# Performance work log

Hardware: AMD Instinct MI355X
Metric: run time of the kernel (lower is better)

Reference implementation:

```python
import math
import jax, jax.numpy as jnp
import numpy as np

NUM_HEADS = 16
D_MODEL = 1024
B, S = 1, 4096


def setup_inputs() -> dict:
    key = jax.random.key(0)
    ks = jax.random.split(key, 10)
    sc = 1.0 / math.sqrt(D_MODEL)
    # causal mask: 1.0 where masked (strictly upper triangular), 0.0 elsewhere
    causal = jnp.triu(jnp.ones((S, S), dtype=jnp.float32), k=1)
    return {
        "query": jax.random.normal(ks[0], (B, S, D_MODEL), dtype=jnp.float32),
        "mask": jnp.broadcast_to(causal, (B, S, S)),
        "Wq": jax.random.normal(ks[1], (D_MODEL, D_MODEL), dtype=jnp.float32) * sc,
        "bq": jax.random.normal(ks[2], (D_MODEL,), dtype=jnp.float32) * sc,
        "Wk": jax.random.normal(ks[3], (D_MODEL, D_MODEL), dtype=jnp.float32) * sc,
        "bk": jax.random.normal(ks[4], (D_MODEL,), dtype=jnp.float32) * sc,
        "Wv": jax.random.normal(ks[5], (D_MODEL, D_MODEL), dtype=jnp.float32) * sc,
        "bv": jax.random.normal(ks[6], (D_MODEL,), dtype=jnp.float32) * sc,
        "Wo": jax.random.normal(ks[7], (D_MODEL, D_MODEL), dtype=jnp.float32) * sc,
        "bo": jax.random.normal(ks[8], (D_MODEL,), dtype=jnp.float32) * sc,
    }


def _split_heads(x, H, dh):
    # [B,S,D] -> [B,H,S,dh]; head h owns channels [h*dh:(h+1)*dh] (matches the
    # module's transpose->reshape->transpose trick, which equals the contiguous split)
    b, s, _ = x.shape
    return x.reshape(b, s, H, dh).transpose(0, 2, 1, 3)


def reference(query, mask, Wq, bq, Wk, bk, Wv, bv, Wo, bo):
    H = NUM_HEADS
    B_, S_, D = query.shape
    dh = D // H
    q = _split_heads(query @ Wq.T + bq, H, dh)   # [B,H,S,dh]
    k = _split_heads(query @ Wk.T + bk, H, dh)   # self-attention: key = query
    v = _split_heads(query @ Wv.T + bv, H, dh)
    # materialized scores [B,H,S,S]
    scores = jnp.einsum("bhqd,bhkd->bhqk", q, k)
    # mask applied BEFORE the 1/sqrt(d_head) scaling, faithful to the source
    scores = scores + mask[:, None, :, :] * (-1e9)
    attn = jax.nn.softmax(scores / math.sqrt(dh), axis=-1)  # [B,H,S,S]
    out = jnp.einsum("bhqk,bhkd->bhqd", attn, v)            # [B,H,S,dh]
    combined = out.transpose(0, 2, 1, 3).reshape(B_, S_, D)  # [B,S,D]
    return combined @ Wo.T + bo
```

## Files before the change

kernel.cpp:

```cpp
#include <hip/hip_runtime.h>

typedef __bf16 bf16x8 __attribute__((ext_vector_type(8)));
typedef __bf16 bf16x4 __attribute__((ext_vector_type(4)));
typedef float f32x4 __attribute__((ext_vector_type(4)));

typedef const __attribute__((address_space(1))) void* as1_cvp;
typedef __attribute__((address_space(3))) void* as3_vp;
__device__ __forceinline__ void g2l16(const void* g, void* l) {
  __builtin_amdgcn_global_load_lds((as1_cvp)(uintptr_t)g, (as3_vp)(uintptr_t)l, 16, 0, 0);
}

__global__ __launch_bounds__(256) void cast_f32_to_bf16(const float* __restrict__ in,
                                                        __bf16* __restrict__ out, int n4) {
  for (int idx = blockIdx.x * 256 + threadIdx.x; idx < n4; idx += gridDim.x * 256) {
    float4 f = reinterpret_cast<const float4*>(in)[idx];
    bf16x4 t;
    t.x = (__bf16)f.x; t.y = (__bf16)f.y; t.z = (__bf16)f.z; t.w = (__bf16)f.w;
    reinterpret_cast<bf16x4*>(out)[idx] = t;
  }
}

__global__ __launch_bounds__(256) void cast3_f32_to_bf16(const float* __restrict__ w0,
                                                         const float* __restrict__ w1,
                                                         const float* __restrict__ w2,
                                                         __bf16* __restrict__ out, int n4,
                                                         float qs) {
  const float* src = blockIdx.y == 0 ? w0 : (blockIdx.y == 1 ? w1 : w2);
  const float s = blockIdx.y == 0 ? qs : 1.0f;
  __bf16* dst = out + (size_t)blockIdx.y * (size_t)n4 * 4;
  for (int idx = blockIdx.x * 256 + threadIdx.x; idx < n4; idx += gridDim.x * 256) {
    float4 f = reinterpret_cast<const float4*>(src)[idx];
    bf16x4 t;
    t.x = (__bf16)(f.x * s); t.y = (__bf16)(f.y * s);
    t.z = (__bf16)(f.z * s); t.w = (__bf16)(f.w * s);
    reinterpret_cast<bf16x4*>(dst)[idx] = t;
  }
}

template <int BM, typename OUT_T, bool VT_FUSE>
__global__ __launch_bounds__(256) void gemm_bt(const __bf16* __restrict__ A,
                                               const __bf16* __restrict__ B,
                                               const float* __restrict__ b0,
                                               const float* __restrict__ b1,
                                               const float* __restrict__ b2,
                                               OUT_T* __restrict__ C,
                                               __bf16* __restrict__ Vt,
                                               int K, int ldc, float qs) {
  constexpr int MT = BM / 32;
  __shared__ __align__(16) __bf16 Alds[BM][64];
  __shared__ __align__(16) __bf16 Blds[128][64];
  const int tid = threadIdx.x;
  const int wave = tid >> 6, lane = tid & 63;
  const int wm = wave & 1, wn = wave >> 1;
  const int mlane = lane & 15, quad = lane >> 4;
  const int m0 = blockIdx.x * BM, n0 = blockIdx.y * 128;

  f32x4 acc[MT][4] = {};
  constexpr int AN = BM * 8 / 256;

  for (int k0 = 0; k0 < K; k0 += 64) {
#pragma unroll
    for (int j = 0; j < AN; j++) {
      int c = j * 256 + tid;
      g2l16(&A[(size_t)(m0 + (c >> 3)) * K + k0 + (c & 7) * 8], &Alds[0][0] + c * 8);
    }
#pragma unroll
    for (int j = 0; j < 4; j++) {
      int c = j * 256 + tid;
      g2l16(&B[(size_t)(n0 + (c >> 3)) * K + k0 + (c & 7) * 8], &Blds[0][0] + c * 8);
    }
    __syncthreads();
    bf16x8 af[MT][2], bfr[4][2];
#pragma unroll
    for (int mt = 0; mt < MT; mt++)
#pragma unroll
      for (int s = 0; s < 2; s++)
        af[mt][s] = *reinterpret_cast<const bf16x8*>(
            &Alds[wm * (BM / 2) + mt * 16 + mlane][s * 32 + quad * 8]);
#pragma unroll
    for (int nt = 0; nt < 4; nt++)
#pragma unroll
      for (int s = 0; s < 2; s++)
        bfr[nt][s] = *reinterpret_cast<const bf16x8*>(
            &Blds[wn * 64 + nt * 16 + mlane][s * 32 + quad * 8]);
#pragma unroll
    for (int mt = 0; mt < MT; mt++)
#pragma unroll
      for (int nt = 0; nt < 4; nt++)
#pragma unroll
        for (int s = 0; s < 2; s++)
          acc[mt][nt] = __builtin_amdgcn_mfma_f32_16x16x32_bf16(af[mt][s], bfr[nt][s],
                                                                acc[mt][nt], 0, 0, 0);
    __syncthreads();
  }

  const int region = n0 >> 10;
  const float* bp = region == 0 ? b0 : (region == 1 ? b1 : b2);
  const float bs = (region == 0) ? qs : 1.0f;
  float bvs[4];
#pragma unroll
  for (int nt = 0; nt < 4; nt++)
    bvs[nt] = bp[(n0 + wn * 64 + nt * 16 + mlane) & 1023] * bs;

  if (VT_FUSE && region == 2) {
#pragma unroll
    for (int mt = 0; mt < MT; mt++)
#pragma unroll
      for (int nt = 0; nt < 4; nt++) {
        int vcol = ((n0 + wn * 64 + nt * 16 + mlane) & 1023);
        int row0 = m0 + wm * (BM / 2) + mt * 16 + quad * 4;
        bf16x4 t;
#pragma unroll
        for (int r = 0; r < 4; r++) t[r] = (__bf16)(acc[mt][nt][r] + bvs[nt]);
        *reinterpret_cast<bf16x4*>(&Vt[(size_t)vcol * 4096 + row0]) = t;
      }
  } else {
#pragma unroll
    for (int mt = 0; mt < MT; mt++)
#pragma unroll
      for (int nt = 0; nt < 4; nt++) {
        int col = n0 + wn * 64 + nt * 16 + mlane;
#pragma unroll
        for (int r = 0; r < 4; r++) {
          int row = m0 + wm * (BM / 2) + mt * 16 + quad * 4 + r;
          C[(size_t)row * ldc + col] = (OUT_T)(acc[mt][nt][r] + bvs[nt]);
        }
      }
  }
}

__global__ __launch_bounds__(512, 4) void flash_attn(const __bf16* __restrict__ QK,
                                                     const __bf16* __restrict__ Vt,
                                                     __bf16* __restrict__ O, int S) {
  const int LDQ = 2048, D = 1024;
  __shared__ __align__(16) __bf16 Klds[128][72];
  __shared__ __align__(16) __bf16 Vlds[64][136];
  __shared__ __align__(16) __bf16 Plds[8][16][72];
  const int tid = threadIdx.x;
  const int wave = tid >> 6, lane = tid & 63;
  const int mlane = lane & 15, quad = lane >> 4;
  const int half = wave >> 2, rw = wave & 3;
  const int b = blockIdx.x, h = blockIdx.y;

  for (int pass = 0; pass < 2; ++pass) {
    const int qb = pass ? b : (63 - b);
    const int qbase = qb * 64 + rw * 16;

    bf16x8 qf[2];
#pragma unroll
    for (int s = 0; s < 2; s++)
      qf[s] = *reinterpret_cast<const bf16x8*>(
          &QK[(size_t)(qbase + mlane) * LDQ + h * 64 + s * 32 + quad * 8]);

    f32x4 o[4] = {};
    float lrow[4] = {0.f, 0.f, 0.f, 0.f};

    const int nkb = qb / 2 + 1;
    for (int kb = 0; kb < nkb; ++kb) {
#pragma unroll
      for (int j = 0; j < 2; j++) {
        int c = j * 512 + tid, r = c >> 3, cc = c & 7;
        *reinterpret_cast<uint4*>(&Klds[r][cc * 8]) = *reinterpret_cast<const uint4*>(
            &QK[(size_t)(kb * 128 + r) * LDQ + 1024 + h * 64 + cc * 8]);
      }
#pragma unroll
      for (int j = 0; j < 2; j++) {
        int c = j * 512 + tid, r = c >> 4, cc = c & 15;
        *reinterpret_cast<uint4*>(&Vlds[r][cc * 8]) = *reinterpret_cast<const uint4*>(
            &Vt[(size_t)(h * 64 + r) * S + kb * 128 + cc * 8]);
      }
      __syncthreads();

      f32x4 sc[4];
#pragma unroll
      for (int nt = 0; nt < 4; nt++) {
        f32x4 a = {};
#pragma unroll
        for (int s = 0; s < 2; s++) {
          bf16x8 bk = *reinterpret_cast<const bf16x8*>(
              &Klds[half * 64 + nt * 16 + mlane][s * 32 + quad * 8]);
          a = __builtin_amdgcn_mfma_f32_16x16x32_bf16(qf[s], bk, a, 0, 0, 0);
        }
        sc[nt] = a;
      }

      const bool maskTile = (kb == nkb - 1);
#pragma unroll
      for (int r = 0; r < 4; r++) {
        if (maskTile) {
          const int qg = qbase + quad * 4 + r;
#pragma unroll
          for (int nt = 0; nt < 4; nt++) {
            int kg = kb * 128 + half * 64 + nt * 16 + mlane;
            if (kg > qg) sc[nt][r] = -INFINITY;
          }
        }
        float ls = 0.f;
#pragma unroll
        for (int nt = 0; nt < 4; nt++) {
          float p = __builtin_amdgcn_exp2f(sc[nt][r]);
          sc[nt][r] = p;
          ls += p;
        }
        lrow[r] += ls;
#pragma unroll
        for (int nt = 0; nt < 4; nt++)
          Plds[wave][quad * 4 + r][nt * 16 + mlane] = (__bf16)sc[nt][r];
      }

#pragma unroll
      for (int s = 0; s < 2; s++) {
        bf16x8 pf =
            *reinterpret_cast<const bf16x8*>(&Plds[wave][mlane][s * 32 + quad * 8]);
#pragma unroll
        for (int nt = 0; nt < 4; nt++) {
          bf16x8 vf = *reinterpret_cast<const bf16x8*>(
              &Vlds[nt * 16 + mlane][half * 64 + s * 32 + quad * 8]);
          o[nt] = __builtin_amdgcn_mfma_f32_16x16x32_bf16(pf, vf, o[nt], 0, 0, 0);
        }
      }
      __syncthreads();
    }

    float* osc = (float*)&Klds[0][0];
    float* lsc = (float*)&Vlds[0][0];
    if (half == 1) {
      const int ob = (rw * 64 + lane) * 18, lb = (rw * 64 + lane) * 5;
#pragma unroll
      for (int nt = 0; nt < 4; nt++)
#pragma unroll
        for (int r = 0; r < 4; r++) osc[ob + nt * 4 + r] = o[nt][r];
#pragma unroll
      for (int r = 0; r < 4; r++) lsc[lb + r] = lrow[r];
    }
    __syncthreads();
    if (half == 0) {
      const int ob = (rw * 64 + lane) * 18, lb = (rw * 64 + lane) * 5;
#pragma unroll
      for (int nt = 0; nt < 4; nt++)
#pragma unroll
        for (int r = 0; r < 4; r++) o[nt][r] += osc[ob + nt * 4 + r];
#pragma unroll
      for (int r = 0; r < 4; r++) {
        float l = lrow[r] + lsc[lb + r];
#pragma unroll
        for (int off = 1; off < 16; off <<= 1) l += __shfl_xor(l, off, 64);
        float inv = 1.0f / l;
        int row = qbase + quad * 4 + r;
#pragma unroll
        for (int nt = 0; nt < 4; nt++)
          O[(size_t)row * D + h * 64 + nt * 16 + mlane] = (__bf16)(o[nt][r] * inv);
      }
    }
    __syncthreads();
  }
}

extern "C" void kernel_launch(void* const* d_in, const int* in_sizes, int n_in,
                              void* d_out, int out_size, void* d_ws, size_t ws_size,
                              hipStream_t stream) {
  const float* query = (const float*)d_in[0];
  const float* Wq = (const float*)d_in[2];
  const float* bq = (const float*)d_in[3];
  const float* Wk = (const float*)d_in[4];
  const float* bk = (const float*)d_in[5];
  const float* Wv = (const float*)d_in[6];
  const float* bv = (const float*)d_in[7];
  const float* Wo = (const float*)d_in[8];
  const float* bo = (const float*)d_in[9];
  float* out = (float*)d_out;

  const int S = 4096, D = 1024;
  const float SCL = 0.125f * 1.44269504088896340736f;
  char* ws = (char*)d_ws;
  __bf16* Xb   = (__bf16*)(ws);
  __bf16* Cb   = (__bf16*)(ws);
  __bf16* Wqkv = (__bf16*)(ws + (8u << 20));
  __bf16* Wob  = (__bf16*)(ws + (14u << 20));
  __bf16* QKb  = (__bf16*)(ws + (16u << 20));
  __bf16* Vt   = (__bf16*)(ws + (32u << 20));

  cast_f32_to_bf16<<<1024, 256, 0, stream>>>(query, Xb, S * D / 4);
  cast3_f32_to_bf16<<<dim3(256, 3), 256, 0, stream>>>(Wq, Wk, Wv, Wqkv, D * D / 4, SCL);
  cast_f32_to_bf16<<<256, 256, 0, stream>>>(Wo, Wob, D * D / 4);

  gemm_bt<128, __bf16, true><<<dim3(S / 128, 3 * D / 128), 256, 0, stream>>>(
      Xb, Wqkv, bq, bk, bv, QKb, Vt, D, 2048, SCL);

  flash_attn<<<dim3(32, 16), 512, 0, stream>>>(QKb, Vt, Cb, S);

  gemm_bt<64, float, false><<<dim3(S / 64, D / 128), 256, 0, stream>>>(
      Cb, Wob, bo, bo, bo, out, nullptr, D, D, 1.0f);
}
```

Measured before the change: 283.5 us.

## Prefetch next K/V tile into registers and retune LDS padding

The attention kernel now loads the next K and V tiles from global memory into registers while the current tile is being computed. At the top of each iteration it only stores those registers into LDS, so global-load latency overlaps with the MFMA and softmax work. The LDS row padding is also cut (72→68, 136→132, reduction stride 18→17) to change the bank mapping. With the new padding, row strides are no longer 16-byte multiples, so the 128-bit LDS accesses may become misaligned. The prefetch also holds extra registers per thread.

```diff
diff --git a/kernel.cpp b/kernel.cpp
--- a/kernel.cpp
+++ b/kernel.cpp
@@ -133,15 +133,18 @@
                                                      const __bf16* __restrict__ Vt,
                                                      __bf16* __restrict__ O, int S) {
   const int LDQ = 2048, D = 1024;
-  __shared__ __align__(16) __bf16 Klds[128][72];
-  __shared__ __align__(16) __bf16 Vlds[64][136];
-  __shared__ __align__(16) __bf16 Plds[8][16][72];
+  __shared__ __align__(16) __bf16 Klds[128][68];
+  __shared__ __align__(16) __bf16 Vlds[64][132];
+  __shared__ __align__(16) __bf16 Plds[8][16][68];
   const int tid = threadIdx.x;
   const int wave = tid >> 6, lane = tid & 63;
   const int mlane = lane & 15, quad = lane >> 4;
   const int half = wave >> 2, rw = wave & 3;
   const int b = blockIdx.x, h = blockIdx.y;
 
+  const int krow = tid >> 3, kcol = (tid & 7) * 8;
+  const int vrow = tid >> 4, vcol = (tid & 15) * 8;
+
   for (int pass = 0; pass < 2; ++pass) {
     const int qb = pass ? b : (63 - b);
     const int qbase = qb * 64 + rw * 16;
@@ -156,20 +159,37 @@
     float lrow[4] = {0.f, 0.f, 0.f, 0.f};
 
     const int nkb = qb / 2 + 1;
+
+    uint4 kreg[2], vreg[2];
+#pragma unroll
+    for (int j = 0; j < 2; j++)
+      kreg[j] = *reinterpret_cast<const uint4*>(
+          &QK[(size_t)(j * 64 + krow) * LDQ + 1024 + h * 64 + kcol]);
+#pragma unroll
+    for (int j = 0; j < 2; j++)
+      vreg[j] = *reinterpret_cast<const uint4*>(
+          &Vt[(size_t)(h * 64 + j * 32 + vrow) * S + vcol]);
+
     for (int kb = 0; kb < nkb; ++kb) {
 #pragma unroll
-      for (int j = 0; j < 2; j++) {
-        int c = j * 512 + tid, r = c >> 3, cc = c & 7;
-        *reinterpret_cast<uint4*>(&Klds[r][cc * 8]) = *reinterpret_cast<const uint4*>(
-            &QK[(size_t)(kb * 128 + r) * LDQ + 1024 + h * 64 + cc * 8]);
-      }
-#pragma unroll
-      for (int j = 0; j < 2; j++) {
-        int c = j * 512 + tid, r = c >> 4, cc = c & 15;
-        *reinterpret_cast<uint4*>(&Vlds[r][cc * 8]) = *reinterpret_cast<const uint4*>(
-            &Vt[(size_t)(h * 64 + r) * S + kb * 128 + cc * 8]);
-      }
+      for (int j = 0; j < 2; j++)
+        *reinterpret_cast<uint4*>(&Klds[j * 64 + krow][kcol]) = kreg[j];
+#pragma unroll
+      for (int j = 0; j < 2; j++)
+        *reinterpret_cast<uint4*>(&Vlds[j * 32 + vrow][vcol]) = vreg[j];
       __syncthreads();
+
+      if (kb + 1 < nkb) {
+        const int kb2 = kb + 1;
+#pragma unroll
+        for (int j = 0; j < 2; j++)
+          kreg[j] = *reinterpret_cast<const uint4*>(
+              &QK[(size_t)(kb2 * 128 + j * 64 + krow) * LDQ + 1024 + h * 64 + kcol]);
+#pragma unroll
+        for (int j = 0; j < 2; j++)
+          vreg[j] = *reinterpret_cast<const uint4*>(
+              &Vt[(size_t)(h * 64 + j * 32 + vrow) * S + kb2 * 128 + vcol]);
+      }
 
       f32x4 sc[4];
 #pragma unroll
@@ -225,7 +245,7 @@
     float* osc = (float*)&Klds[0][0];
     float* lsc = (float*)&Vlds[0][0];
     if (half == 1) {
-      const int ob = (rw * 64 + lane) * 18, lb = (rw * 64 + lane) * 5;
+      const int ob = (rw * 64 + lane) * 17, lb = (rw * 64 + lane) * 5;
 #pragma unroll
       for (int nt = 0; nt < 4; nt++)
 #pragma unroll
@@ -235,7 +255,7 @@
     }
     __syncthreads();
     if (half == 0) {
-      const int ob = (rw * 64 + lane) * 18, lb = (rw * 64 + lane) * 5;
+      const int ob = (rw * 64 + lane) * 17, lb = (rw * 64 + lane) * 5;
 #pragma unroll
       for (int nt = 0; nt < 4; nt++)
 #pragma unroll
```

New measurement: 369.9 us. +30.5%, slower.
